# Optimization experiments

Hardware: AMD Instinct MI355X
Metric: run time of the kernel (lower is better)

Reference implementation:

```python
import jax, jax.numpy as jnp
import numpy as np

N = 50000      # num_nodes
E = 800000     # num_edges (avg degree 16)
D = 128        # embedding_dim
HID = 32       # per-head hidden dim of conv1
H = 8          # heads of conv1
OUT = 128      # output_dim


def setup_inputs() -> dict:
    key = jax.random.key(0)
    ks = jax.random.split(key, 14)
    s = lambda fan_in: 1.0 / np.sqrt(fan_in)
    return {
        "x": jax.random.randint(ks[0], (N,), 0, N),
        "edge_index": jax.random.randint(ks[1], (2, E), 0, N),
        "emb": jax.random.normal(ks[2], (N, D), jnp.float32),
        # conv1: GATConv(D, HID, heads=H, concat=True)
        "W1": jax.random.normal(ks[3], (D, H * HID), jnp.float32) * s(D),
        "a_src1": jax.random.normal(ks[4], (H, HID), jnp.float32) * s(HID),
        "a_dst1": jax.random.normal(ks[5], (H, HID), jnp.float32) * s(HID),
        "b1": jnp.zeros((H * HID,), jnp.float32),
        # conv2: GATConv(H*HID, OUT, heads=1, concat=False)
        "W2": jax.random.normal(ks[6], (H * HID, OUT), jnp.float32) * s(H * HID),
        "a_src2": jax.random.normal(ks[7], (1, OUT), jnp.float32) * s(OUT),
        "a_dst2": jax.random.normal(ks[8], (1, OUT), jnp.float32) * s(OUT),
        "b2": jnp.zeros((OUT,), jnp.float32),
        # output Linear(OUT, OUT)
        "Wo": jax.random.normal(ks[9], (OUT, OUT), jnp.float32) * s(OUT),
        "bo": jnp.zeros((OUT,), jnp.float32),
    }


def _segment_softmax(e, seg, n):
    # e: [E, H]; softmax over edges sharing the same destination node
    m = jax.ops.segment_max(e, seg, num_segments=n)            # [N, H]
    ex = jnp.exp(e - m[seg])
    denom = jax.ops.segment_sum(ex, seg, num_segments=n)       # [N, H]
    return ex / (denom[seg] + 1e-16)


def _gat_conv(x, src, dst, W, a_src, a_dst, b, concat):
    n = x.shape[0]
    Hh, C = a_src.shape
    h = (x @ W).reshape(n, Hh, C)                              # [N, H, C]
    al_src = (h * a_src).sum(-1)                               # [N, H]
    al_dst = (h * a_dst).sum(-1)                               # [N, H]
    e = jax.nn.leaky_relu(al_src[src] + al_dst[dst], 0.2)      # [E, H]
    alpha = _segment_softmax(e, dst, n)                        # [E, H]
    out = jax.ops.segment_sum(h[src] * alpha[:, :, None], dst, num_segments=n)
    out = out.reshape(n, Hh * C) if concat else out.mean(axis=1)
    return out + b


def reference(x, edge_index, emb, W1, a_src1, a_dst1, b1,
              W2, a_src2, a_dst2, b2, Wo, bo):
    n = x.shape[0]
    loops = jnp.arange(n)
    src = jnp.concatenate([edge_index[0], loops])              # add self-loops (PyG default)
    dst = jnp.concatenate([edge_index[1], loops])
    h = emb[x]                                                 # [N, D]
    h = _gat_conv(h, src, dst, W1, a_src1, a_dst1, b1, concat=True)
    h = _gat_conv(h, src, dst, W2, a_src2, a_dst2, b2, concat=False)
    return h @ Wo + bo
```

## Files before the change

### kernel.cpp

```cpp
#include <hip/hip_runtime.h>
#include <hip/hip_bf16.h>

#define NN 50000
#define EE 800000
#define DD 128
#define F1 256
#define F2 128

using short8  = __attribute__((ext_vector_type(8))) short;
using floatx4 = __attribute__((ext_vector_type(4))) float;

__device__ inline float bf2f(ushort u) { return __uint_as_float(((unsigned)u) << 16); }
__device__ inline ushort f2bf(float f) {
    unsigned u = __float_as_uint(f);
    u += 0x7fffu + ((u >> 16) & 1u);
    return (ushort)(u >> 16);
}

#define HB ((EE + 255) / 256)
#define GB ((NN + 1) / 2)
#define W1B ((DD * F1 + 255) / 256)
#define W2B ((F1 * F2 + 255) / 256)
#define WOB ((F2 * F2 + 255) / 256)

__global__ __launch_bounds__(256) void k_prep(
    const int* __restrict__ edst, int* __restrict__ cnt,
    const int* __restrict__ x, const float* __restrict__ emb, ushort* __restrict__ Ax,
    const float* __restrict__ W1, ushort* __restrict__ W1t,
    const float* __restrict__ W2, ushort* __restrict__ W2t,
    const float* __restrict__ Wo, ushort* __restrict__ Wot) {
    int b = blockIdx.x;
    if (b < HB) {
        int i = b * 256 + threadIdx.x;
        if (i < EE) atomicAdd(&cnt[edst[i]], 1);
    } else if (b < HB + GB) {
        int row = (b - HB) * 2 + (threadIdx.x >> 7);
        if (row < NN) {
            int c = threadIdx.x & 127;
            Ax[(size_t)row * DD + c] = f2bf(emb[(size_t)x[row] * DD + c]);
        }
    } else if (b < HB + GB + W1B) {
        int idx = (b - HB - GB) * 256 + threadIdx.x;
        int k = idx / F1, n = idx % F1;
        W1t[(size_t)n * DD + k] = f2bf(W1[(size_t)k * F1 + n]);
    } else if (b < HB + GB + W1B + W2B) {
        int idx = (b - HB - GB - W1B) * 256 + threadIdx.x;
        int k = idx / F2, n = idx % F2;
        W2t[(size_t)n * F1 + k] = f2bf(W2[(size_t)k * F2 + n]);
    } else {
        int idx = (b - HB - GB - W1B - W2B) * 256 + threadIdx.x;
        int k = idx / F2, n = idx % F2;
        Wot[(size_t)n * F2 + k] = f2bf(Wo[(size_t)k * F2 + n]);
    }
}

__global__ void k_scan1(const int* __restrict__ cnt, int* __restrict__ out,
                        int* __restrict__ sums) {
    __shared__ int s[256];
    int i = blockIdx.x * 256 + threadIdx.x;
    int v = (i < NN) ? cnt[i] + 1 : 0;
    s[threadIdx.x] = v;
    __syncthreads();
    for (int off = 1; off < 256; off <<= 1) {
        int t = (threadIdx.x >= off) ? s[threadIdx.x - off] : 0;
        __syncthreads();
        s[threadIdx.x] += t;
        __syncthreads();
    }
    if (i < NN) out[i] = s[threadIdx.x] - v;
    if (threadIdx.x == 255) sums[blockIdx.x] = s[255];
}

__global__ void k_scan3(int* __restrict__ offsets, const int* __restrict__ sums,
                        int* __restrict__ cursor, int nb) {
    __shared__ int s[256];
    int v = (threadIdx.x < nb) ? sums[threadIdx.x] : 0;
    s[threadIdx.x] = v;
    __syncthreads();
    for (int off = 1; off < 256; off <<= 1) {
        int t = (threadIdx.x >= off) ? s[threadIdx.x - off] : 0;
        __syncthreads();
        s[threadIdx.x] += t;
        __syncthreads();
    }
    int base = (blockIdx.x == 0) ? 0 : s[blockIdx.x - 1];
    int i = blockIdx.x * 256 + threadIdx.x;
    if (i < NN) {
        int o = offsets[i] + base;
        offsets[i] = o;
        cursor[i] = o;
    }
    if (blockIdx.x == 0 && threadIdx.x == 0) offsets[NN] = EE + NN;
}

__global__ void k_scatter(const int* __restrict__ esrc, const int* __restrict__ edst,
                          int* __restrict__ cursor, int* __restrict__ srcs) {
    int i = blockIdx.x * 256 + threadIdx.x;
    if (i < EE) {
        int pos = atomicAdd(&cursor[edst[i]], 1);
        srcs[pos] = esrc[i];
    } else if (i < EE + NN) {
        int n = i - EE;
        int pos = atomicAdd(&cursor[n], 1);
        srcs[pos] = n;
    }
}

template<int K, int MODE>
__global__ __launch_bounds__(256, 2) void k_mfma_gemm(
    const ushort* __restrict__ A, const ushort* __restrict__ Bt,
    void* __restrict__ Cout, int ldc, const float* __restrict__ bias,
    const float* __restrict__ avs, const float* __restrict__ avd,
    float* __restrict__ out_s, float* __restrict__ out_d) {
    __shared__ ushort As[128][72];
    __shared__ ushort Bs[128][72];
    __shared__ float als[2][128], ald[2][128];
    const int t    = threadIdx.x;
    const int lane = t & 63;
    const int w    = t >> 6;
    const int wr   = w >> 1, wc = w & 1;
    const int m0   = blockIdx.x * 128;
    const int n0   = blockIdx.y * 128;
    floatx4 acc[4][4] = {};
    for (int k0 = 0; k0 < K; k0 += 64) {
        #pragma unroll
        for (int p = 0; p < 4; ++p) {
            int linear = p * 2048 + t * 8;
            int row = linear >> 6;
            int col = linear & 63;
            short8 va = {};
            int gm = m0 + row;
            if (gm < NN) va = *(const short8*)(A + (size_t)gm * K + k0 + col);
            *(short8*)&As[row][col] = va;
            short8 vb = *(const short8*)(Bt + (size_t)(n0 + row) * K + k0 + col);
            *(short8*)&Bs[row][col] = vb;
        }
        __syncthreads();
        #pragma unroll
        for (int kk = 0; kk < 64; kk += 32) {
            const int q8 = (lane >> 4) * 8;
            short8 af[4], bf[4];
            #pragma unroll
            for (int i = 0; i < 4; ++i)
                af[i] = *(const short8*)&As[wr * 64 + i * 16 + (lane & 15)][kk + q8];
            #pragma unroll
            for (int j = 0; j < 4; ++j)
                bf[j] = *(const short8*)&Bs[wc * 64 + j * 16 + (lane & 15)][kk + q8];
            #pragma unroll
            for (int i = 0; i < 4; ++i)
                #pragma unroll
                for (int j = 0; j < 4; ++j)
                    acc[i][j] = __builtin_amdgcn_mfma_f32_16x16x32_bf16(
                        af[i], bf[j], acc[i][j], 0, 0, 0);
        }
        __syncthreads();
    }
    const int q  = lane >> 4;
    const int r0 = q * 4;
    const int cc = lane & 15;
    float as0, as1, as2, as3, ad0, ad1, ad2, ad3;
    if (MODE == 1 || MODE == 2) {
        as0 = avs[n0 + wc * 64 +  0 + cc]; ad0 = avd[n0 + wc * 64 +  0 + cc];
        as1 = avs[n0 + wc * 64 + 16 + cc]; ad1 = avd[n0 + wc * 64 + 16 + cc];
        as2 = avs[n0 + wc * 64 + 32 + cc]; ad2 = avd[n0 + wc * 64 + 32 + cc];
        as3 = avs[n0 + wc * 64 + 48 + cc]; ad3 = avd[n0 + wc * 64 + 48 + cc];
    }
    #pragma unroll
    for (int i = 0; i < 4; ++i) {
        #pragma unroll
        for (int r = 0; r < 4; ++r) {
            int m = m0 + wr * 64 + i * 16 + r0 + r;
            if (MODE == 1) {
                float hs0 = acc[i][0][r] * as0 + acc[i][1][r] * as1;
                float hs1 = acc[i][2][r] * as2 + acc[i][3][r] * as3;
                float hd0 = acc[i][0][r] * ad0 + acc[i][1][r] * ad1;
                float hd1 = acc[i][2][r] * ad2 + acc[i][3][r] * ad3;
                #pragma unroll
                for (int mask = 1; mask < 16; mask <<= 1) {
                    hs0 += __shfl_xor(hs0, mask);
                    hs1 += __shfl_xor(hs1, mask);
                    hd0 += __shfl_xor(hd0, mask);
                    hd1 += __shfl_xor(hd1, mask);
                }
                if (cc == 0 && m < NN) {
                    int gh = (n0 >> 5) + wc * 2;
                    out_s[m * 8 + gh] = hs0;   out_s[m * 8 + gh + 1] = hs1;
                    out_d[m * 8 + gh] = hd0;   out_d[m * 8 + gh + 1] = hd1;
                }
            }
            if (MODE == 2) {
                float ps = acc[i][0][r] * as0 + acc[i][1][r] * as1
                         + acc[i][2][r] * as2 + acc[i][3][r] * as3;
                float pd = acc[i][0][r] * ad0 + acc[i][1][r] * ad1
                         + acc[i][2][r] * ad2 + acc[i][3][r] * ad3;
                #pragma unroll
                for (int mask = 1; mask < 16; mask <<= 1) {
                    ps += __shfl_xor(ps, mask);
                    pd += __shfl_xor(pd, mask);
                }
                if (cc == 0) {
                    int lr = wr * 64 + i * 16 + r0 + r;
                    als[wc][lr] = ps;
                    ald[wc][lr] = pd;
                }
            }
            if (m < NN) {
                #pragma unroll
                for (int j = 0; j < 4; ++j) {
                    int n = n0 + wc * 64 + j * 16 + cc;
                    float v = acc[i][j][r];
                    if (MODE == 3) ((float*)Cout)[(size_t)m * ldc + n] = v + bias[n];
                    else           ((ushort*)Cout)[(size_t)m * ldc + n] = f2bf(v);
                }
            }
        }
    }
    if (MODE == 2) {
        __syncthreads();
        if (t < 128) {
            int m = m0 + t;
            if (m < NN) {
                out_s[m] = als[0][t] + als[1][t];
                out_d[m] = ald[0][t] + ald[1][t];
            }
        }
    }
}

__device__ inline float lrelu(float x) { return x > 0.f ? x : 0.2f * x; }

__global__ __launch_bounds__(256) void k_agg1(
    const int* __restrict__ offsets, const int* __restrict__ srcs,
    const ushort* __restrict__ h1, const float* __restrict__ a1s,
    const float* __restrict__ a1d, const float* __restrict__ b1,
    ushort* __restrict__ out1) {
    __shared__ float atab[4][512];
    __shared__ int   stab[4][64];
    const int w = threadIdx.x >> 6;
    const int d = blockIdx.x * 4 + w;
    if (d >= NN) return;
    const int lane = threadIdx.x & 63;
    const int beg = offsets[d], end = offsets[d + 1];
    const int e8 = lane >> 3, h8 = lane & 7;
    const float ad = a1d[d * 8 + h8];
    float m = -1e30f, den = 0.f;
    for (int i = beg + e8; i < end; i += 8) {
        int s = srcs[i];
        float v = lrelu(a1s[s * 8 + h8] + ad);
        float nm = fmaxf(m, v);
        den = den * __expf(m - nm) + __expf(v - nm);
        m = nm;
    }
    #pragma unroll
    for (int mask = 8; mask < 64; mask <<= 1) {
        float om = __shfl_xor(m, mask);
        float od = __shfl_xor(den, mask);
        float nm = fmaxf(m, om);
        den = den * __expf(m - nm) + od * __expf(om - nm);
        m = nm;
    }
    float rden = 1.f / (den + 1e-16f);
    float4 acc = make_float4(0.f, 0.f, 0.f, 0.f);
    const int hh = lane >> 3;
    for (int tb = beg; tb < end; tb += 64) {
        int cnt = min(64, end - tb);
        if (lane < cnt) stab[w][lane] = srcs[tb + lane];
        int np = cnt * 8;
        for (int p = lane; p < np; p += 64) {
            int s = stab[w][p >> 3];
            float v = lrelu(a1s[s * 8 + h8] + ad);
            atab[w][p] = __expf(v - m) * rden;
        }
        int e = 0;
        for (; e + 4 <= cnt; e += 4) {
            int s0 = stab[w][e], s1 = stab[w][e + 1];
            int s2 = stab[w][e + 2], s3 = stab[w][e + 3];
            ushort4 u0 = *(const ushort4*)(h1 + (size_t)s0 * F1 + lane * 4);
            ushort4 u1 = *(const ushort4*)(h1 + (size_t)s1 * F1 + lane * 4);
            ushort4 u2 = *(const ushort4*)(h1 + (size_t)s2 * F1 + lane * 4);
            ushort4 u3 = *(const ushort4*)(h1 + (size_t)s3 * F1 + lane * 4);
            float a0 = atab[w][(e + 0) * 8 + hh];
            float a1 = atab[w][(e + 1) * 8 + hh];
            float a2 = atab[w][(e + 2) * 8 + hh];
            float a3 = atab[w][(e + 3) * 8 + hh];
            acc.x += a0 * bf2f(u0.x) + a1 * bf2f(u1.x) + a2 * bf2f(u2.x) + a3 * bf2f(u3.x);
            acc.y += a0 * bf2f(u0.y) + a1 * bf2f(u1.y) + a2 * bf2f(u2.y) + a3 * bf2f(u3.y);
            acc.z += a0 * bf2f(u0.z) + a1 * bf2f(u1.z) + a2 * bf2f(u2.z) + a3 * bf2f(u3.z);
            acc.w += a0 * bf2f(u0.w) + a1 * bf2f(u1.w) + a2 * bf2f(u2.w) + a3 * bf2f(u3.w);
        }
        for (; e < cnt; ++e) {
            int s = stab[w][e];
            float alpha = atab[w][e * 8 + hh];
            ushort4 u = *(const ushort4*)(h1 + (size_t)s * F1 + lane * 4);
            acc.x += alpha * bf2f(u.x); acc.y += alpha * bf2f(u.y);
            acc.z += alpha * bf2f(u.z); acc.w += alpha * bf2f(u.w);
        }
    }
    float4 bb = *(const float4*)(b1 + lane * 4);
    ushort4 o;
    o.x = f2bf(acc.x + bb.x); o.y = f2bf(acc.y + bb.y);
    o.z = f2bf(acc.z + bb.z); o.w = f2bf(acc.w + bb.w);
    *(ushort4*)(out1 + (size_t)d * F1 + lane * 4) = o;
}

__global__ __launch_bounds__(256) void k_agg2(
    const int* __restrict__ offsets, const int* __restrict__ srcs,
    const ushort* __restrict__ h2, const float* __restrict__ a2s,
    const float* __restrict__ a2d, const float* __restrict__ b2,
    ushort* __restrict__ out2) {
    __shared__ float atab[4][64];
    __shared__ int   stab[4][64];
    const int w = threadIdx.x >> 6;
    const int d = blockIdx.x * 4 + w;
    if (d >= NN) return;
    const int lane = threadIdx.x & 63;
    const int beg = offsets[d], end = offsets[d + 1];
    const float ad = a2d[d];
    float m = -1e30f, den = 0.f;
    for (int i = beg + lane; i < end; i += 64) {
        int s = srcs[i];
        float v = lrelu(a2s[s] + ad);
        float nm = fmaxf(m, v);
        den = den * __expf(m - nm) + __expf(v - nm);
        m = nm;
    }
    #pragma unroll
    for (int mask = 1; mask < 64; mask <<= 1) {
        float om = __shfl_xor(m, mask);
        float od = __shfl_xor(den, mask);
        float nm = fmaxf(m, om);
        den = den * __expf(m - nm) + od * __expf(om - nm);
        m = nm;
    }
    float rden = 1.f / (den + 1e-16f);
    float2 acc = make_float2(0.f, 0.f);
    for (int tb = beg; tb < end; tb += 64) {
        int cnt = min(64, end - tb);
        if (lane < cnt) {
            int s = srcs[tb + lane];
            stab[w][lane] = s;
            atab[w][lane] = __expf(lrelu(a2s[s] + ad) - m) * rden;
        }
        int e = 0;
        for (; e + 4 <= cnt; e += 4) {
            int s0 = stab[w][e], s1 = stab[w][e + 1];
            int s2 = stab[w][e + 2], s3 = stab[w][e + 3];
            ushort2 u0 = *(const ushort2*)(h2 + (size_t)s0 * F2 + lane * 2);
            ushort2 u1 = *(const ushort2*)(h2 + (size_t)s1 * F2 + lane * 2);
            ushort2 u2 = *(const ushort2*)(h2 + (size_t)s2 * F2 + lane * 2);
            ushort2 u3 = *(const ushort2*)(h2 + (size_t)s3 * F2 + lane * 2);
            float a0 = atab[w][e + 0], a1 = atab[w][e + 1];
            float a2 = atab[w][e + 2], a3 = atab[w][e + 3];
            acc.x += a0 * bf2f(u0.x) + a1 * bf2f(u1.x) + a2 * bf2f(u2.x) + a3 * bf2f(u3.x);
            acc.y += a0 * bf2f(u0.y) + a1 * bf2f(u1.y) + a2 * bf2f(u2.y) + a3 * bf2f(u3.y);
        }
        for (; e < cnt; ++e) {
            int s = stab[w][e];
            float alpha = atab[w][e];
            ushort2 u = *(const ushort2*)(h2 + (size_t)s * F2 + lane * 2);
            acc.x += alpha * bf2f(u.x); acc.y += alpha * bf2f(u.y);
        }
    }
    float2 bb = *(const float2*)(b2 + lane * 2);
    ushort2 o;
    o.x = f2bf(acc.x + bb.x); o.y = f2bf(acc.y + bb.y);
    *(ushort2*)(out2 + (size_t)d * F2 + lane * 2) = o;
}

extern "C" void kernel_launch(void* const* d_in, const int* in_sizes, int n_in,
                              void* d_out, int out_size, void* d_ws, size_t ws_size,
                              hipStream_t stream) {
    const int*   x      = (const int*)d_in[0];
    const int*   edge   = (const int*)d_in[1];
    const float* emb    = (const float*)d_in[2];
    const float* W1     = (const float*)d_in[3];
    const float* a_src1 = (const float*)d_in[4];
    const float* a_dst1 = (const float*)d_in[5];
    const float* b1     = (const float*)d_in[6];
    const float* W2     = (const float*)d_in[7];
    const float* a_src2 = (const float*)d_in[8];
    const float* a_dst2 = (const float*)d_in[9];
    const float* b2     = (const float*)d_in[10];
    const float* Wo     = (const float*)d_in[11];
    const float* bo     = (const float*)d_in[12];
    float* out = (float*)d_out;

    char* w = (char*)d_ws;
    auto alloc = [&](size_t bytes) {
        char* p = w;
        w += (bytes + 255) & ~(size_t)255;
        return p;
    };
    int*    offsets = (int*)alloc((NN + 1) * sizeof(int));
    int*    cursor  = (int*)alloc(NN * sizeof(int));
    int*    sums    = (int*)alloc(256 * sizeof(int));
    int*    srcs    = (int*)alloc((size_t)(EE + NN) * sizeof(int));
    ushort* Ax      = (ushort*)alloc((size_t)NN * DD * sizeof(ushort));
    ushort* W1t     = (ushort*)alloc((size_t)DD * F1 * sizeof(ushort));
    ushort* W2t     = (ushort*)alloc((size_t)F1 * F2 * sizeof(ushort));
    ushort* Wot     = (ushort*)alloc((size_t)F2 * F2 * sizeof(ushort));
    ushort* h1      = (ushort*)alloc((size_t)NN * F1 * sizeof(ushort));
    ushort* out1    = (ushort*)alloc((size_t)NN * F1 * sizeof(ushort));
    ushort* h2      = (ushort*)alloc((size_t)NN * F2 * sizeof(ushort));
    ushort* out2    = (ushort*)alloc((size_t)NN * F2 * sizeof(ushort));
    float*  a1s     = (float*)alloc((size_t)NN * 8 * sizeof(float));
    float*  a1d     = (float*)alloc((size_t)NN * 8 * sizeof(float));
    float*  a2s     = a1s;
    float*  a2d     = a1d;

    const int* esrc = edge;
    const int* edst = edge + EE;

    const int NB = (NN + 255) / 256;

    hipMemsetAsync(cursor, 0, NN * sizeof(int), stream);
    k_prep<<<HB + GB + W1B + W2B + WOB, 256, 0, stream>>>(
        edst, cursor, x, emb, Ax, W1, W1t, W2, W2t, Wo, Wot);
    k_scan1<<<NB, 256, 0, stream>>>(cursor, offsets, sums);
    k_scan3<<<NB, 256, 0, stream>>>(offsets, sums, cursor, NB);
    k_scatter<<<(EE + NN + 255) / 256, 256, 0, stream>>>(esrc, edst, cursor, srcs);

    const int MT = (NN + 127) / 128;

    k_mfma_gemm<DD, 1><<<dim3(MT, F1 / 128), 256, 0, stream>>>(
        Ax, W1t, h1, F1, nullptr, a_src1, a_dst1, a1s, a1d);
    k_agg1<<<(NN + 3) / 4, 256, 0, stream>>>(offsets, srcs, h1, a1s, a1d, b1, out1);

    k_mfma_gemm<F1, 2><<<dim3(MT, 1), 256, 0, stream>>>(
        out1, W2t, h2, F2, nullptr, a_src2, a_dst2, a2s, a2d);
    k_agg2<<<(NN + 3) / 4, 256, 0, stream>>>(offsets, srcs, h2, a2s, a2d, b2, out2);

    k_mfma_gemm<F2, 3><<<dim3(MT, 1), 256, 0, stream>>>(
        out2, Wot, out, F2, bo, nullptr, nullptr, nullptr, nullptr);
}
```

Before: 366.4 us.

## Apply output linear before layer-2 aggregation and fold biases; unroll gathers by 8

Aggregation is linear, so the output projection Wo is applied to h2 ahead of the layer-2 aggregation, and b2·Wo+bo is precomputed into a combined bias. The aggregation kernel then writes the final fp32 output directly, which removes the separate final GEMM's read of an intermediate and the bf16 round-trip of out2. The gather loops in both aggregation kernels are also unrolled from 4 to 8 edges so more loads are in flight. The price is an extra bf16 rounding of h2·Wo before aggregation and more register pressure from the wider unroll.

Result: no change. 369.3 us (+0.8%).

```diff
diff --git a/kernel.cpp b/kernel.cpp
--- a/kernel.cpp
+++ b/kernel.cpp
@@ -28,7 +28,9 @@
     const int* __restrict__ x, const float* __restrict__ emb, ushort* __restrict__ Ax,
     const float* __restrict__ W1, ushort* __restrict__ W1t,
     const float* __restrict__ W2, ushort* __restrict__ W2t,
-    const float* __restrict__ Wo, ushort* __restrict__ Wot) {
+    const float* __restrict__ Wo, ushort* __restrict__ Wot,
+    const float* __restrict__ b2, const float* __restrict__ bo,
+    float* __restrict__ bc) {
     int b = blockIdx.x;
     if (b < HB) {
         int i = b * 256 + threadIdx.x;
@@ -47,10 +49,17 @@
         int idx = (b - HB - GB - W1B) * 256 + threadIdx.x;
         int k = idx / F2, n = idx % F2;
         W2t[(size_t)n * F1 + k] = f2bf(W2[(size_t)k * F2 + n]);
-    } else {
+    } else if (b < HB + GB + W1B + W2B + WOB) {
         int idx = (b - HB - GB - W1B - W2B) * 256 + threadIdx.x;
         int k = idx / F2, n = idx % F2;
         Wot[(size_t)n * F2 + k] = f2bf(Wo[(size_t)k * F2 + n]);
+    } else {
+        int j = threadIdx.x;
+        if (j < F2) {
+            float s = bo[j];
+            for (int k = 0; k < F2; ++k) s += b2[k] * Wo[(size_t)k * F2 + j];
+            bc[j] = s;
+        }
     }
 }
 
@@ -158,7 +167,7 @@
     const int q  = lane >> 4;
     const int r0 = q * 4;
     const int cc = lane & 15;
-    float as0, as1, as2, as3, ad0, ad1, ad2, ad3;
+    float as0 = 0, as1 = 0, as2 = 0, as3 = 0, ad0 = 0, ad1 = 0, ad2 = 0, ad3 = 0;
     if (MODE == 1 || MODE == 2) {
         as0 = avs[n0 + wc * 64 +  0 + cc]; ad0 = avd[n0 + wc * 64 +  0 + cc];
         as1 = avs[n0 + wc * 64 + 16 + cc]; ad1 = avd[n0 + wc * 64 + 16 + cc];
@@ -208,9 +217,7 @@
                 #pragma unroll
                 for (int j = 0; j < 4; ++j) {
                     int n = n0 + wc * 64 + j * 16 + cc;
-                    float v = acc[i][j][r];
-                    if (MODE == 3) ((float*)Cout)[(size_t)m * ldc + n] = v + bias[n];
-                    else           ((ushort*)Cout)[(size_t)m * ldc + n] = f2bf(v);
+                    ((ushort*)Cout)[(size_t)m * ldc + n] = f2bf(acc[i][j][r]);
                 }
             }
         }
@@ -272,21 +279,21 @@
             atab[w][p] = __expf(v - m) * rden;
         }
         int e = 0;
-        for (; e + 4 <= cnt; e += 4) {
-            int s0 = stab[w][e], s1 = stab[w][e + 1];
-            int s2 = stab[w][e + 2], s3 = stab[w][e + 3];
-            ushort4 u0 = *(const ushort4*)(h1 + (size_t)s0 * F1 + lane * 4);
-            ushort4 u1 = *(const ushort4*)(h1 + (size_t)s1 * F1 + lane * 4);
-            ushort4 u2 = *(const ushort4*)(h1 + (size_t)s2 * F1 + lane * 4);
-            ushort4 u3 = *(const ushort4*)(h1 + (size_t)s3 * F1 + lane * 4);
-            float a0 = atab[w][(e + 0) * 8 + hh];
-            float a1 = atab[w][(e + 1) * 8 + hh];
-            float a2 = atab[w][(e + 2) * 8 + hh];
-            float a3 = atab[w][(e + 3) * 8 + hh];
-            acc.x += a0 * bf2f(u0.x) + a1 * bf2f(u1.x) + a2 * bf2f(u2.x) + a3 * bf2f(u3.x);
-            acc.y += a0 * bf2f(u0.y) + a1 * bf2f(u1.y) + a2 * bf2f(u2.y) + a3 * bf2f(u3.y);
-            acc.z += a0 * bf2f(u0.z) + a1 * bf2f(u1.z) + a2 * bf2f(u2.z) + a3 * bf2f(u3.z);
-            acc.w += a0 * bf2f(u0.w) + a1 * bf2f(u1.w) + a2 * bf2f(u2.w) + a3 * bf2f(u3.w);
+        for (; e + 8 <= cnt; e += 8) {
+            ushort4 u[8]; float a[8];
+            #pragma unroll
+            for (int jj = 0; jj < 8; ++jj) {
+                int s = stab[w][e + jj];
+                u[jj] = *(const ushort4*)(h1 + (size_t)s * F1 + lane * 4);
+                a[jj] = atab[w][(e + jj) * 8 + hh];
+            }
+            #pragma unroll
+            for (int jj = 0; jj < 8; ++jj) {
+                acc.x += a[jj] * bf2f(u[jj].x);
+                acc.y += a[jj] * bf2f(u[jj].y);
+                acc.z += a[jj] * bf2f(u[jj].z);
+                acc.w += a[jj] * bf2f(u[jj].w);
+            }
         }
         for (; e < cnt; ++e) {
             int s = stab[w][e];
@@ -305,9 +312,9 @@
 
 __global__ __launch_bounds__(256) void k_agg2(
     const int* __restrict__ offsets, const int* __restrict__ srcs,
-    const ushort* __restrict__ h2, const float* __restrict__ a2s,
-    const float* __restrict__ a2d, const float* __restrict__ b2,
-    ushort* __restrict__ out2) {
+    const ushort* __restrict__ h3, const float* __restrict__ a2s,
+    const float* __restrict__ a2d, const float* __restrict__ bc,
+    float* __restrict__ out) {
     __shared__ float atab[4][64];
     __shared__ int   stab[4][64];
     const int w = threadIdx.x >> 6;
@@ -342,29 +349,29 @@
             atab[w][lane] = __expf(lrelu(a2s[s] + ad) - m) * rden;
         }
         int e = 0;
-        for (; e + 4 <= cnt; e += 4) {
-            int s0 = stab[w][e], s1 = stab[w][e + 1];
-            int s2 = stab[w][e + 2], s3 = stab[w][e + 3];
-            ushort2 u0 = *(const ushort2*)(h2 + (size_t)s0 * F2 + lane * 2);
-            ushort2 u1 = *(const ushort2*)(h2 + (size_t)s1 * F2 + lane * 2);
-            ushort2 u2 = *(const ushort2*)(h2 + (size_t)s2 * F2 + lane * 2);
-            ushort2 u3 = *(const ushort2*)(h2 + (size_t)s3 * F2 + lane * 2);
-            float a0 = atab[w][e + 0], a1 = atab[w][e + 1];
-            float a2 = atab[w][e + 2], a3 = atab[w][e + 3];
-            acc.x += a0 * bf2f(u0.x) + a1 * bf2f(u1.x) + a2 * bf2f(u2.x) + a3 * bf2f(u3.x);
-            acc.y += a0 * bf2f(u0.y) + a1 * bf2f(u1.y) + a2 * bf2f(u2.y) + a3 * bf2f(u3.y);
+        for (; e + 8 <= cnt; e += 8) {
+            ushort2 u[8]; float a[8];
+            #pragma unroll
+            for (int jj = 0; jj < 8; ++jj) {
+                int s = stab[w][e + jj];
+                u[jj] = *(const ushort2*)(h3 + (size_t)s * F2 + lane * 2);
+                a[jj] = atab[w][e + jj];
+            }
+            #pragma unroll
+            for (int jj = 0; jj < 8; ++jj) {
+                acc.x += a[jj] * bf2f(u[jj].x);
+                acc.y += a[jj] * bf2f(u[jj].y);
+            }
         }
         for (; e < cnt; ++e) {
             int s = stab[w][e];
             float alpha = atab[w][e];
-            ushort2 u = *(const ushort2*)(h2 + (size_t)s * F2 + lane * 2);
+            ushort2 u = *(const ushort2*)(h3 + (size_t)s * F2 + lane * 2);
             acc.x += alpha * bf2f(u.x); acc.y += alpha * bf2f(u.y);
         }
     }
-    float2 bb = *(const float2*)(b2 + lane * 2);
-    ushort2 o;
-    o.x = f2bf(acc.x + bb.x); o.y = f2bf(acc.y + bb.y);
-    *(ushort2*)(out2 + (size_t)d * F2 + lane * 2) = o;
+    float2 bb = *(const float2*)(bc + lane * 2);
+    *(float2*)(out + (size_t)d * F2 + lane * 2) = make_float2(acc.x + bb.x, acc.y + bb.y);
 }
 
 extern "C" void kernel_launch(void* const* d_in, const int* in_sizes, int n_in,
@@ -402,9 +409,10 @@
     ushort* h1      = (ushort*)alloc((size_t)NN * F1 * sizeof(ushort));
     ushort* out1    = (ushort*)alloc((size_t)NN * F1 * sizeof(ushort));
     ushort* h2      = (ushort*)alloc((size_t)NN * F2 * sizeof(ushort));
-    ushort* out2    = (ushort*)alloc((size_t)NN * F2 * sizeof(ushort));
+    ushort* h3      = (ushort*)alloc((size_t)NN * F2 * sizeof(ushort));
     float*  a1s     = (float*)alloc((size_t)NN * 8 * sizeof(float));
     float*  a1d     = (float*)alloc((size_t)NN * 8 * sizeof(float));
+    float*  bc      = (float*)alloc(F2 * sizeof(float));
     float*  a2s     = a1s;
     float*  a2d     = a1d;
 
@@ -414,8 +422,8 @@
     const int NB = (NN + 255) / 256;
 
     hipMemsetAsync(cursor, 0, NN * sizeof(int), stream);
-    k_prep<<<HB + GB + W1B + W2B + WOB, 256, 0, stream>>>(
-        edst, cursor, x, emb, Ax, W1, W1t, W2, W2t, Wo, Wot);
+    k_prep<<<HB + GB + W1B + W2B + WOB + 1, 256, 0, stream>>>(
+        edst, cursor, x, emb, Ax, W1, W1t, W2, W2t, Wo, Wot, b2, bo, bc);
     k_scan1<<<NB, 256, 0, stream>>>(cursor, offsets, sums);
     k_scan3<<<NB, 256, 0, stream>>>(offsets, sums, cursor, NB);
     k_scatter<<<(EE + NN + 255) / 256, 256, 0, stream>>>(esrc, edst, cursor, srcs);
@@ -428,8 +436,9 @@
 
     k_mfma_gemm<F1, 2><<<dim3(MT, 1), 256, 0, stream>>>(
         out1, W2t, h2, F2, nullptr, a_src2, a_dst2, a2s, a2d);
-    k_agg2<<<(NN + 3) / 4, 256, 0, stream>>>(offsets, srcs, h2, a2s, a2d, b2, out2);
-
-    k_mfma_gemm<F2, 3><<<dim3(MT, 1), 256, 0, stream>>>(
-        out2, Wot, out, F2, bo, nullptr, nullptr, nullptr, nullptr);
-}
+
+    k_mfma_gemm<F2, 0><<<dim3(MT, 1), 256, 0, stream>>>(
+        h2, Wot, h3, F2, nullptr, nullptr, nullptr, nullptr, nullptr);
+
+    k_agg2<<<(NN + 3) / 4, 256, 0, stream>>>(offsets, srcs, h3, a2s, a2d, bc, out);
+}
```
